# Performance work log

Hardware: AMD Instinct MI355X
Metric: run time of the kernel (lower is better)

Reference implementation:

```python
import jax, jax.numpy as jnp
import numpy as np

BN_EPS = 1e-5
NN_CHUNK = 1024  # unknown points processed per distance-matrix tile


def _batch_ids(cnt, total):
    # contiguous per-batch layout -> batch id of each point via cumsum/searchsorted
    return jnp.searchsorted(jnp.cumsum(cnt), jnp.arange(total), side='right')


def three_nn(unknown, known, ub_id, kb_id):
    """Ragged brute-force 3-NN. Returns (squared dists [N,3], global idx [N,3])."""
    N = unknown.shape[0]
    nchunk = N // NN_CHUNK
    u = unknown.reshape(nchunk, NN_CHUNK, 3)
    ub = ub_id.reshape(nchunk, NN_CHUNK)

    def body(args):
        uc, bc = args
        d2 = jnp.sum((uc[:, None, :] - known[None, :, :]) ** 2, axis=-1)  # [chunk, M]
        d2 = jnp.where(bc[:, None] == kb_id[None, :], d2, jnp.inf)  # mask cross-batch pairs
        neg_d, idx = jax.lax.top_k(-d2, 3)
        return -neg_d, idx

    d2, idx = jax.lax.map(body, (u, ub))
    return d2.reshape(N, 3), idx.reshape(N, 3)


def three_interpolate(known_feats, idx, weight):
    # gather [N,3,C] then inverse-distance weighted sum -> [N,C]
    gathered = known_feats[idx]  # [N,3,C]
    return jnp.einsum('nkc,nk->nc', gathered, weight)


def conv_bn_relu(x, W, gamma, beta):
    # 1x1 Conv2d over [1,C,N,1] == pointwise matmul; BN (training stats) over points
    h = x @ W.T  # [N, C_out]
    mean = jnp.mean(h, axis=0)
    var = jnp.mean((h - mean) ** 2, axis=0)  # biased, as torch BN normalization
    h = (h - mean) * jax.lax.rsqrt(var + BN_EPS) * gamma + beta
    return jax.nn.relu(h)


def setup_inputs() -> dict:
    key = jax.random.key(0)
    ks = jax.random.split(key, 10)
    B, Nper, Mper, C1, C2 = 4, 16384, 4096, 128, 256
    N, M = B * Nper, B * Mper
    unknown = jax.random.normal(ks[0], (N, 3), jnp.float32) * 10.0
    known = jax.random.normal(ks[1], (M, 3), jnp.float32) * 10.0
    unknown_feats = jax.random.normal(ks[2], (N, C1), jnp.float32)
    known_feats = jax.random.normal(ks[3], (M, C2), jnp.float32)
    unknown_batch_cnt = jnp.full((B,), Nper, jnp.int32)
    known_batch_cnt = jnp.full((B,), Mper, jnp.int32)
    Cin = C1 + C2  # 384
    W1 = jax.random.normal(ks[4], (256, Cin), jnp.float32) * (1.0 / np.sqrt(Cin))
    W2 = jax.random.normal(ks[5], (256, 256), jnp.float32) * (1.0 / np.sqrt(256))
    g1 = jnp.ones((256,), jnp.float32); b1 = jnp.zeros((256,), jnp.float32)
    g2 = jnp.ones((256,), jnp.float32); b2 = jnp.zeros((256,), jnp.float32)
    return {"unknown": unknown, "unknown_batch_cnt": unknown_batch_cnt,
            "known": known, "known_batch_cnt": known_batch_cnt,
            "unknown_feats": unknown_feats, "known_feats": known_feats,
            "W1": W1, "g1": g1, "b1": b1, "W2": W2, "g2": g2, "b2": b2}


def reference(unknown, unknown_batch_cnt, known, known_batch_cnt,
              unknown_feats, known_feats, W1, g1, b1, W2, g2, b2):
    ub_id = _batch_ids(unknown_batch_cnt, unknown.shape[0])
    kb_id = _batch_ids(known_batch_cnt, known.shape[0])
    dist, idx = three_nn(unknown, known, ub_id, kb_id)  # squared dists, as CUDA kernel
    dist_recip = 1.0 / (dist + 1e-8)
    weight = dist_recip / jnp.sum(dist_recip, axis=-1, keepdims=True)
    interpolated = three_interpolate(known_feats, idx, weight)  # [N, C2]
    new_features = jnp.concatenate([interpolated, unknown_feats], axis=1)  # [N, C2+C1]
    new_features = conv_bn_relu(new_features, W1, g1, b1)
    new_features = conv_bn_relu(new_features, W2, g2, b2)
    return new_features  # [N, 256]
```

## Files before the change

### kernel.cpp

```cpp
#include <hip/hip_runtime.h>
#include <math.h>

typedef __attribute__((ext_vector_type(8))) short short8;
typedef __attribute__((ext_vector_type(4))) float f32x4;

#define INF 3.0e38f
#define BN_EPS 1e-5f

__device__ __forceinline__ unsigned short f2bf(float x) {
    union { float f; unsigned u; } v; v.f = x;
    unsigned r = v.u + 0x7FFF + ((v.u >> 16) & 1);
    return (unsigned short)(r >> 16);
}
__device__ __forceinline__ float bf2f(unsigned short u) {
    return __uint_as_float(((unsigned)u) << 16);
}

__global__ __launch_bounds__(256) void knn3_kernel(
    const float* __restrict__ unk, const float* __restrict__ kn,
    const int* __restrict__ ucnt, const int* __restrict__ kcnt,
    int B, int N, float* __restrict__ wgt, int* __restrict__ idxo)
{
    __shared__ float md[4][64][3];
    __shared__ float d2g[64];
    __shared__ unsigned long long mk[4][64][3];

    int tid = threadIdx.x;
    int s = __builtin_amdgcn_readfirstlane(tid >> 6);
    int lane = tid & 63;
    int pbase = blockIdx.x * 64;
    int p = pbase + lane;

    int cum = 0, bb = 0;
    for (int i = 0; i < B; i++) { int c = ucnt[i]; if (pbase >= cum) bb = i; cum += c; }
    int kstart = 0;
    for (int i = 0; i < bb; i++) kstart += kcnt[i];
    int kend = kstart + kcnt[bb];

    float ux = unk[p * 3 + 0], uy = unk[p * 3 + 1], uz = unk[p * 3 + 2];

    int qlen = (kend - kstart) >> 2;
    int jbase = kstart + s * qlen;
    const float* kq = kn + (size_t)jbase * 3;

    float d0 = INF, d1 = INF, d2 = INF;
    auto upd = [&](float e) {
        float m0 = fmaxf(e, d0);
        float m1 = fmaxf(e, d1);
        d0 = fminf(e, d0);
        d1 = fminf(m0, d1);
        d2 = fminf(m1, d2);
    };

    for (int i = 0; i < qlen; i += 8) {
        float e[8];
#pragma unroll
        for (int c = 0; c < 8; c++) {
            float kx = kq[(i + c) * 3 + 0];
            float ky = kq[(i + c) * 3 + 1];
            float kz = kq[(i + c) * 3 + 2];
            float dx = kx - ux, dy = ky - uy, dz = kz - uz;
            e[c] = __builtin_fmaf(dx, dx, __builtin_fmaf(dy, dy, dz * dz));
        }
#pragma unroll
        for (int c = 0; c < 8; c++) upd(e[c]);
    }

    md[s][lane][0] = d0; md[s][lane][1] = d1; md[s][lane][2] = d2;
    __syncthreads();
    if (tid < 64) {
        float v0 = INF, v1 = INF, v2 = INF;
#pragma unroll
        for (int w = 0; w < 4; w++)
#pragma unroll
            for (int k = 0; k < 3; k++) {
                float e = md[w][tid][k];
                float m0 = fmaxf(e, v0);
                float m1 = fmaxf(e, v1);
                v0 = fminf(e, v0);
                v1 = fminf(m0, v1);
                v2 = fminf(m1, v2);
            }
        d2g[tid] = v2;
    }
    __syncthreads();
    float thr = d2g[lane];

    unsigned long long s0 = ~0ULL, s1 = ~0ULL, s2 = ~0ULL;
    auto insK = [&](unsigned long long k) {
        bool c0 = k < s0;
        unsigned long long t0 = c0 ? k : s0;
        unsigned long long t1 = c0 ? s0 : k;
        bool c1 = t1 < s1;
        unsigned long long u0 = c1 ? t1 : s1;
        unsigned long long u1 = c1 ? s1 : t1;
        s0 = t0; s1 = u0;
        s2 = u1 < s2 ? u1 : s2;
    };
    auto mkkey = [](float e, int gj) {
        return ((unsigned long long)__float_as_uint(e) << 32) | (unsigned)gj;
    };

    for (int i = 0; i < qlen; i += 4) {
        float e[4];
#pragma unroll
        for (int c = 0; c < 4; c++) {
            float kx = kq[(i + c) * 3 + 0];
            float ky = kq[(i + c) * 3 + 1];
            float kz = kq[(i + c) * 3 + 2];
            float dx = kx - ux, dy = ky - uy, dz = kz - uz;
            e[c] = __builtin_fmaf(dx, dx, __builtin_fmaf(dy, dy, dz * dz));
        }
        float m4 = fminf(fminf(e[0], e[1]), fminf(e[2], e[3]));
        if (m4 <= thr) {
            int gj = jbase + i;
            insK(mkkey(e[0], gj + 0));
            insK(mkkey(e[1], gj + 1));
            insK(mkkey(e[2], gj + 2));
            insK(mkkey(e[3], gj + 3));
        }
    }

    mk[s][lane][0] = s0; mk[s][lane][1] = s1; mk[s][lane][2] = s2;
    __syncthreads();

    if (tid < 64) {
        s0 = s1 = s2 = ~0ULL;
#pragma unroll
        for (int qq = 0; qq < 4; qq++)
#pragma unroll
            for (int kk = 0; kk < 3; kk++)
                insK(mk[qq][tid][kk]);

        float dd0 = __uint_as_float((unsigned)(s0 >> 32));
        float dd1 = __uint_as_float((unsigned)(s1 >> 32));
        float dd2 = __uint_as_float((unsigned)(s2 >> 32));
        float r0 = 1.0f / (dd0 + 1e-8f);
        float r1 = 1.0f / (dd1 + 1e-8f);
        float r2 = 1.0f / (dd2 + 1e-8f);
        float rs = 1.0f / (r0 + r1 + r2);
        int pp = pbase + tid;
        wgt[pp * 3 + 0] = r0 * rs;
        wgt[pp * 3 + 1] = r1 * rs;
        wgt[pp * 3 + 2] = r2 * rs;
        idxo[pp * 3 + 0] = (int)(unsigned)s0;
        idxo[pp * 3 + 1] = (int)(unsigned)s1;
        idxo[pp * 3 + 2] = (int)(unsigned)s2;
    }
}

__global__ __launch_bounds__(256) void wconv_kernel(
    const float* __restrict__ W1, const float* __restrict__ W2,
    unsigned short* __restrict__ W1b, unsigned short* __restrict__ W2b,
    int n1, int n2)
{
    int i = blockIdx.x * 256 + threadIdx.x;
    if (i < n1) W1b[i] = f2bf(W1[i]);
    int j = i - n1;
    if (j >= 0 && j < n2) W2b[j] = f2bf(W2[j]);
}

template <int K, int MODE>
__global__ __launch_bounds__(256) void gemm_bf16_kernel(
    const void* __restrict__ Aa, const float* __restrict__ ufeat,
    const unsigned short* __restrict__ W,
    const float* __restrict__ wgt, const int* __restrict__ idxv,
    const float* __restrict__ bnsum, const float* __restrict__ bnsq,
    const float* __restrict__ bng, const float* __restrict__ bnb, float invN,
    void* __restrict__ Cv, float* __restrict__ gsum, float* __restrict__ gsq)
{
    __shared__ unsigned short As[128 * 40];
    __shared__ unsigned short Bs[128 * 40];
    __shared__ float colsum[128];
    __shared__ float colsq[128];
    __shared__ float sc[256], sh[256];

    int tid = threadIdx.x;
    int w = tid >> 6, lane = tid & 63;
    int r = w >> 1, cq = w & 1;
    int m16 = lane & 15, q = lane >> 4;
    int bm = blockIdx.x * 128, bn = blockIdx.y * 128;

    if (MODE == 1) {
        float mean = bnsum[tid] * invN;
        float var = bnsq[tid] * invN - mean * mean;
        float scv = bng[tid] * rsqrtf(var + BN_EPS);
        sc[tid] = scv;
        sh[tid] = bnb[tid] - mean * scv;
    }

    int srow = tid >> 2;
    int kc = (tid & 3) * 8;
    float w0a[2], w1a[2], w2a[2];
    int j0a[2], j1a[2], j2a[2];
    if (MODE == 2) {
#pragma unroll
        for (int t = 0; t < 2; t++) {
            int pp = bm + srow + 64 * t;
            w0a[t] = wgt[pp * 3 + 0]; w1a[t] = wgt[pp * 3 + 1]; w2a[t] = wgt[pp * 3 + 2];
            j0a[t] = idxv[pp * 3 + 0]; j1a[t] = idxv[pp * 3 + 1]; j2a[t] = idxv[pp * 3 + 2];
        }
    }

    f32x4 acc[4][4];
#pragma unroll
    for (int i = 0; i < 4; i++)
#pragma unroll
        for (int j = 0; j < 4; j++) acc[i][j] = (f32x4){0.f, 0.f, 0.f, 0.f};

#pragma unroll
    for (int k0 = 0; k0 < K; k0 += 32) {
        __syncthreads();
#pragma unroll
        for (int t = 0; t < 2; t++) {
            int row = srow + 64 * t;
            int c = k0 + kc;
            ushort4 o0, o1;
            if (MODE == 2) {
                if (c < 256) {
                    const float* f0 = (const float*)Aa + (size_t)j0a[t] * 256 + c;
                    const float* f1 = (const float*)Aa + (size_t)j1a[t] * 256 + c;
                    const float* f2 = (const float*)Aa + (size_t)j2a[t] * 256 + c;
                    float4 x0 = *(const float4*)f0, x1 = *(const float4*)(f0 + 4);
                    float4 y0 = *(const float4*)f1, y1 = *(const float4*)(f1 + 4);
                    float4 z0 = *(const float4*)f2, z1 = *(const float4*)(f2 + 4);
                    float W0 = w0a[t], W1 = w1a[t], W2 = w2a[t];
                    o0.x = f2bf(x0.x * W0 + y0.x * W1 + z0.x * W2);
                    o0.y = f2bf(x0.y * W0 + y0.y * W1 + z0.y * W2);
                    o0.z = f2bf(x0.z * W0 + y0.z * W1 + z0.z * W2);
                    o0.w = f2bf(x0.w * W0 + y0.w * W1 + z0.w * W2);
                    o1.x = f2bf(x1.x * W0 + y1.x * W1 + z1.x * W2);
                    o1.y = f2bf(x1.y * W0 + y1.y * W1 + z1.y * W2);
                    o1.z = f2bf(x1.z * W0 + y1.z * W1 + z1.z * W2);
                    o1.w = f2bf(x1.w * W0 + y1.w * W1 + z1.w * W2);
                } else {
                    const float* fu = ufeat + (size_t)(bm + row) * 128 + (c - 256);
                    float4 u0 = *(const float4*)fu, u1 = *(const float4*)(fu + 4);
                    o0.x = f2bf(u0.x); o0.y = f2bf(u0.y);
                    o0.z = f2bf(u0.z); o0.w = f2bf(u0.w);
                    o1.x = f2bf(u1.x); o1.y = f2bf(u1.y);
                    o1.z = f2bf(u1.z); o1.w = f2bf(u1.w);
                }
            } else {
                const unsigned short* Ab = (const unsigned short*)Aa;
                ushort4 h0 = *(const ushort4*)(Ab + (size_t)(bm + row) * K + c);
                ushort4 h1v = *(const ushort4*)(Ab + (size_t)(bm + row) * K + c + 4);
                float4 s0 = *(const float4*)&sc[c];
                float4 s1 = *(const float4*)&sc[c + 4];
                float4 t0 = *(const float4*)&sh[c];
                float4 t1 = *(const float4*)&sh[c + 4];
                o0.x = f2bf(fmaxf(bf2f(h0.x) * s0.x + t0.x, 0.f));
                o0.y = f2bf(fmaxf(bf2f(h0.y) * s0.y + t0.y, 0.f));
                o0.z = f2bf(fmaxf(bf2f(h0.z) * s0.z + t0.z, 0.f));
                o0.w = f2bf(fmaxf(bf2f(h0.w) * s0.w + t0.w, 0.f));
                o1.x = f2bf(fmaxf(bf2f(h1v.x) * s1.x + t1.x, 0.f));
                o1.y = f2bf(fmaxf(bf2f(h1v.y) * s1.y + t1.y, 0.f));
                o1.z = f2bf(fmaxf(bf2f(h1v.z) * s1.z + t1.z, 0.f));
                o1.w = f2bf(fmaxf(bf2f(h1v.w) * s1.w + t1.w, 0.f));
            }
            *(ushort4*)&As[row * 40 + kc] = o0;
            *(ushort4*)&As[row * 40 + kc + 4] = o1;
            *(short8*)&Bs[row * 40 + kc] =
                *(const short8*)(W + (size_t)(bn + row) * K + k0 + kc);
        }
        __syncthreads();

        short8 af[4], bf[4];
#pragma unroll
        for (int sub = 0; sub < 4; sub++) {
            af[sub] = *(const short8*)&As[(r * 64 + sub * 16 + m16) * 40 + q * 8];
            bf[sub] = *(const short8*)&Bs[(cq * 64 + sub * 16 + m16) * 40 + q * 8];
        }
#pragma unroll
        for (int sm = 0; sm < 4; sm++)
#pragma unroll
            for (int sn = 0; sn < 4; sn++)
                acc[sm][sn] = __builtin_amdgcn_mfma_f32_16x16x32_bf16(
                    af[sm], bf[sn], acc[sm][sn], 0, 0, 0);
    }

    int row0 = bm + r * 64 + q * 4;
    int col0 = bn + cq * 64 + m16;
#pragma unroll
    for (int sm = 0; sm < 4; sm++)
#pragma unroll
        for (int sn = 0; sn < 4; sn++) {
            f32x4 v = acc[sm][sn];
#pragma unroll
            for (int reg = 0; reg < 4; reg++) {
                size_t idx = (size_t)(row0 + sm * 16 + reg) * 256 + col0 + sn * 16;
                if (MODE == 2) ((unsigned short*)Cv)[idx] = f2bf(v[reg]);
                else           ((float*)Cv)[idx] = v[reg];
            }
        }

    __syncthreads();
    if (tid < 128) { colsum[tid] = 0.f; colsq[tid] = 0.f; }
    __syncthreads();
#pragma unroll
    for (int sn = 0; sn < 4; sn++) {
        float sacc = 0.f, qacc = 0.f;
#pragma unroll
        for (int sm = 0; sm < 4; sm++) {
            f32x4 v = acc[sm][sn];
#pragma unroll
            for (int reg = 0; reg < 4; reg++) {
                sacc += v[reg];
                qacc += v[reg] * v[reg];
            }
        }
        int lc = cq * 64 + sn * 16 + m16;
        atomicAdd(&colsum[lc], sacc);
        atomicAdd(&colsq[lc], qacc);
    }
    __syncthreads();
    if (tid < 128) {
        atomicAdd(&gsum[bn + tid], colsum[tid]);
        atomicAdd(&gsq[bn + tid], colsq[tid]);
    }
}

__global__ __launch_bounds__(256) void final_act_kernel(
    const float* __restrict__ h2, const float* __restrict__ bnsum,
    const float* __restrict__ bnsq, const float* __restrict__ bng,
    const float* __restrict__ bnb, float invN,
    float* __restrict__ out, int total4)
{
    __shared__ float sc[256], sh[256];
    int c = threadIdx.x;
    float mean = bnsum[c] * invN;
    float var = bnsq[c] * invN - mean * mean;
    float scv = bng[c] * rsqrtf(var + BN_EPS);
    sc[c] = scv;
    sh[c] = bnb[c] - mean * scv;
    __syncthreads();

    int i = blockIdx.x * 256 + threadIdx.x;
    if (i >= total4) return;
    int c4 = i & 63;
    float4 v = ((const float4*)h2)[i];
    float4 s = *(const float4*)&sc[c4 * 4];
    float4 t = *(const float4*)&sh[c4 * 4];
    float4 o;
    o.x = fmaxf(v.x * s.x + t.x, 0.0f);
    o.y = fmaxf(v.y * s.y + t.y, 0.0f);
    o.z = fmaxf(v.z * s.z + t.z, 0.0f);
    o.w = fmaxf(v.w * s.w + t.w, 0.0f);
    ((float4*)out)[i] = o;
}

extern "C" void kernel_launch(void* const* d_in, const int* in_sizes, int n_in,
                              void* d_out, int out_size, void* d_ws, size_t ws_size,
                              hipStream_t stream)
{
    const float* unknown = (const float*)d_in[0];
    const int*   ucnt    = (const int*)d_in[1];
    const float* known   = (const float*)d_in[2];
    const int*   kcnt    = (const int*)d_in[3];
    const float* ufeat   = (const float*)d_in[4];
    const float* kfeat   = (const float*)d_in[5];
    const float* W1      = (const float*)d_in[6];
    const float* g1      = (const float*)d_in[7];
    const float* b1      = (const float*)d_in[8];
    const float* W2      = (const float*)d_in[9];
    const float* g2      = (const float*)d_in[10];
    const float* b2      = (const float*)d_in[11];

    int N = in_sizes[0] / 3;
    int B = in_sizes[1];

    char* ws = (char*)d_ws;
    size_t off = 0;
    float* wgt = (float*)(ws + off);            off += (size_t)N * 3 * 4;
    int*   idxb = (int*)(ws + off);             off += (size_t)N * 3 * 4;
    float* stats = (float*)(ws + off);          off += 4 * 256 * 4;
    float* sum1 = stats,        *sq1 = stats + 256;
    float* sum2 = stats + 512,  *sq2 = stats + 768;
    unsigned short* W1b = (unsigned short*)(ws + off);  off += 256 * 384 * 2;
    unsigned short* W2b = (unsigned short*)(ws + off);  off += 256 * 256 * 2;
    off = (off + 255) & ~(size_t)255;
    unsigned short* h1 = (unsigned short*)(ws + off);   off += (size_t)N * 256 * 2;
    off = (off + 255) & ~(size_t)255;
    float* h2 = (float*)(ws + off);

    float invN = 1.0f / (float)N;

    hipMemsetAsync(stats, 0, 4 * 256 * 4, stream);

    wconv_kernel<<<(256 * 384 + 256 * 256 + 255) / 256, 256, 0, stream>>>(
        W1, W2, W1b, W2b, 256 * 384, 256 * 256);
    knn3_kernel<<<N / 64, 256, 0, stream>>>(unknown, known, ucnt, kcnt,
                                            B, N, wgt, idxb);
    gemm_bf16_kernel<384, 2><<<dim3(N / 128, 2), 256, 0, stream>>>(
        kfeat, ufeat, W1b, wgt, idxb,
        nullptr, nullptr, nullptr, nullptr, 0.f, h1, sum1, sq1);
    gemm_bf16_kernel<256, 1><<<dim3(N / 128, 2), 256, 0, stream>>>(
        h1, nullptr, W2b, nullptr, nullptr,
        sum1, sq1, g1, b1, invN, h2, sum2, sq2);
    final_act_kernel<<<N / 4, 256, 0, stream>>>(h2, sum2, sq2, g2, b2, invN,
                                                (float*)d_out, N * 64);
}
```

Before: 393.0 us.

## Replace brute-force 3-NN with x-sorted bucket search and pruned sweep

Known points are bucketed by x coordinate per batch through a histogram, a prefix scan and an atomic scatter into a sorted float4 array. Each query then sweeps outward left and right from its bucket using four lanes, pruning once the x-distance exceeds the current third-best bound, which is shared among the lanes by shuffles. This replaces the two full brute-force passes over every known point in the batch. It adds three small kernels and divergent while loops, and the bucket range is hardcoded to [-64, 64], so points outside it are clamped into the edge buckets.

```diff
diff --git a/kernel.cpp b/kernel.cpp
--- a/kernel.cpp
+++ b/kernel.cpp
@@ -6,6 +6,12 @@
 
 #define INF 3.0e38f
 #define BN_EPS 1e-5f
+
+#define NB 1024
+#define XMIN (-64.0f)
+#define XMAX (64.0f)
+#define BW 0.125f
+#define INVW 8.0f
 
 __device__ __forceinline__ unsigned short f2bf(float x) {
     union { float f; unsigned u; } v; v.f = x;
@@ -16,125 +22,153 @@
     return __uint_as_float(((unsigned)u) << 16);
 }
 
-__global__ __launch_bounds__(256) void knn3_kernel(
-    const float* __restrict__ unk, const float* __restrict__ kn,
-    const int* __restrict__ ucnt, const int* __restrict__ kcnt,
-    int B, int N, float* __restrict__ wgt, int* __restrict__ idxo)
-{
-    __shared__ float md[4][64][3];
-    __shared__ float d2g[64];
-    __shared__ unsigned long long mk[4][64][3];
-
+__global__ __launch_bounds__(256) void hist_kernel(
+    const float* __restrict__ kn, const int* __restrict__ kcnt,
+    int B, int M, int* __restrict__ cnt)
+{
+    int j = blockIdx.x * 256 + threadIdx.x;
+    if (j >= M) return;
+    int cum = 0, bb = 0;
+    for (int i = 0; i < B; i++) { int c = kcnt[i]; if (j >= cum) bb = i; cum += c; }
+    float x = kn[j * 3];
+    int bi = (int)((x - XMIN) * INVW);
+    bi = min(max(bi, 0), NB - 1);
+    atomicAdd(&cnt[bb * NB + bi], 1);
+}
+
+__global__ __launch_bounds__(1024) void scan_kernel(
+    const int* __restrict__ cnt, int* __restrict__ bs, int* __restrict__ cur, int T)
+{
+    __shared__ int ts[1024];
     int tid = threadIdx.x;
-    int s = __builtin_amdgcn_readfirstlane(tid >> 6);
-    int lane = tid & 63;
+    int base = tid * 4;
+    int v0 = 0, v1 = 0, v2 = 0, v3 = 0;
+    if (base + 0 < T) v0 = cnt[base + 0];
+    if (base + 1 < T) v1 = cnt[base + 1];
+    if (base + 2 < T) v2 = cnt[base + 2];
+    if (base + 3 < T) v3 = cnt[base + 3];
+    int s = v0 + v1 + v2 + v3;
+    ts[tid] = s;
+    __syncthreads();
+    for (int off = 1; off < 1024; off <<= 1) {
+        int t = (tid >= off) ? ts[tid - off] : 0;
+        __syncthreads();
+        ts[tid] += t;
+        __syncthreads();
+    }
+    int ex = ts[tid] - s;
+    if (base + 0 < T) { bs[base + 0] = ex; cur[base + 0] = ex; } ex += v0;
+    if (base + 1 < T) { bs[base + 1] = ex; cur[base + 1] = ex; } ex += v1;
+    if (base + 2 < T) { bs[base + 2] = ex; cur[base + 2] = ex; } ex += v2;
+    if (base + 3 < T) { bs[base + 3] = ex; cur[base + 3] = ex; } ex += v3;
+    if (tid == ((T - 1) >> 2)) bs[T] = ts[tid];
+}
+
+__global__ __launch_bounds__(256) void scatter_kernel(
+    const float* __restrict__ kn, const int* __restrict__ kcnt,
+    int B, int M, int* __restrict__ cur, float4* __restrict__ scat)
+{
+    int j = blockIdx.x * 256 + threadIdx.x;
+    if (j >= M) return;
+    int cum = 0, bb = 0;
+    for (int i = 0; i < B; i++) { int c = kcnt[i]; if (j >= cum) bb = i; cum += c; }
+    float x = kn[j * 3], y = kn[j * 3 + 1], z = kn[j * 3 + 2];
+    int bi = (int)((x - XMIN) * INVW);
+    bi = min(max(bi, 0), NB - 1);
+    int pos = atomicAdd(&cur[bb * NB + bi], 1);
+    scat[pos] = make_float4(x, y, z, __int_as_float(j));
+}
+
+__global__ __launch_bounds__(256) void knn3_grid_kernel(
+    const float* __restrict__ unk, const int* __restrict__ ucnt,
+    const int* __restrict__ bs, const float4* __restrict__ scat,
+    int B, float* __restrict__ wgt, int* __restrict__ idxo)
+{
+    __shared__ unsigned long long mk[64][4][3];
+
+    int tid = threadIdx.x;
+    int lp = tid >> 2;
+    int role = tid & 3;
     int pbase = blockIdx.x * 64;
-    int p = pbase + lane;
+    int p = pbase + lp;
 
     int cum = 0, bb = 0;
     for (int i = 0; i < B; i++) { int c = ucnt[i]; if (pbase >= cum) bb = i; cum += c; }
-    int kstart = 0;
-    for (int i = 0; i < bb; i++) kstart += kcnt[i];
-    int kend = kstart + kcnt[bb];
 
     float ux = unk[p * 3 + 0], uy = unk[p * 3 + 1], uz = unk[p * 3 + 2];
 
-    int qlen = (kend - kstart) >> 2;
-    int jbase = kstart + s * qlen;
-    const float* kq = kn + (size_t)jbase * 3;
-
-    float d0 = INF, d1 = INF, d2 = INF;
-    auto upd = [&](float e) {
-        float m0 = fmaxf(e, d0);
-        float m1 = fmaxf(e, d1);
-        d0 = fminf(e, d0);
-        d1 = fminf(m0, d1);
-        d2 = fminf(m1, d2);
+    int kst = bs[bb * NB];
+    int ken = bs[(bb + 1) * NB];
+    int bq = (int)((ux - XMIN) * INVW);
+    bq = min(max(bq, 0), NB - 1);
+    int sp = bs[bb * NB + bq];
+
+    bool left = (role < 2);
+    int sub = role & 1;
+    int pos = left ? (sp - 1 - sub) : (sp + sub);
+    int step = left ? -2 : 2;
+
+    unsigned long long k0 = ~0ULL, k1 = ~0ULL, k2 = ~0ULL;
+    auto insK = [&](unsigned long long k) {
+        bool c0 = k < k0;
+        unsigned long long t0 = c0 ? k : k0;
+        unsigned long long t1 = c0 ? k0 : k;
+        bool c1 = t1 < k1;
+        unsigned long long u0 = c1 ? t1 : k1;
+        unsigned long long u1 = c1 ? k1 : t1;
+        k0 = t0; k1 = u0;
+        k2 = u1 < k2 ? u1 : k2;
     };
 
-    for (int i = 0; i < qlen; i += 8) {
-        float e[8];
-#pragma unroll
-        for (int c = 0; c < 8; c++) {
-            float kx = kq[(i + c) * 3 + 0];
-            float ky = kq[(i + c) * 3 + 1];
-            float kz = kq[(i + c) * 3 + 2];
-            float dx = kx - ux, dy = ky - uy, dz = kz - uz;
-            e[c] = __builtin_fmaf(dx, dx, __builtin_fmaf(dy, dy, dz * dz));
-        }
-#pragma unroll
-        for (int c = 0; c < 8; c++) upd(e[c]);
-    }
-
-    md[s][lane][0] = d0; md[s][lane][1] = d1; md[s][lane][2] = d2;
-    __syncthreads();
+    float Bnd = INF;
+    bool alive = left ? (pos >= kst) : (pos < ken);
+    int it = 0;
+    while (__any(alive)) {
+        if (alive) {
+            float4 f = scat[pos];
+            float dx = f.x - ux, dy = f.y - uy, dz = f.z - uz;
+            float e = __builtin_fmaf(dx, dx, __builtin_fmaf(dy, dy, dz * dz));
+            if (e <= Bnd) {
+                insK(((unsigned long long)__float_as_uint(e) << 32) |
+                     (unsigned)__float_as_int(f.w));
+                Bnd = fminf(Bnd, __uint_as_float((unsigned)(k2 >> 32)));
+            }
+            float xc = left ? fmaxf(f.x, XMIN) : fminf(f.x, XMAX);
+            float t = (left ? (ux - xc) : (xc - ux)) - BW;
+            if (t > 0.0f && t * t >= Bnd) alive = false;
+            pos += step;
+            if (left ? (pos < kst) : (pos >= ken)) alive = false;
+        }
+        if ((++it & 7) == 0) {
+            float b = fminf(Bnd, __shfl_xor(Bnd, 1));
+            Bnd = fminf(b, __shfl_xor(b, 2));
+        }
+    }
+
+    mk[lp][role][0] = k0; mk[lp][role][1] = k1; mk[lp][role][2] = k2;
+    __syncthreads();
+
     if (tid < 64) {
-        float v0 = INF, v1 = INF, v2 = INF;
-#pragma unroll
-        for (int w = 0; w < 4; w++)
-#pragma unroll
-            for (int k = 0; k < 3; k++) {
-                float e = md[w][tid][k];
-                float m0 = fmaxf(e, v0);
-                float m1 = fmaxf(e, v1);
-                v0 = fminf(e, v0);
-                v1 = fminf(m0, v1);
-                v2 = fminf(m1, v2);
-            }
-        d2g[tid] = v2;
-    }
-    __syncthreads();
-    float thr = d2g[lane];
-
-    unsigned long long s0 = ~0ULL, s1 = ~0ULL, s2 = ~0ULL;
-    auto insK = [&](unsigned long long k) {
-        bool c0 = k < s0;
-        unsigned long long t0 = c0 ? k : s0;
-        unsigned long long t1 = c0 ? s0 : k;
-        bool c1 = t1 < s1;
-        unsigned long long u0 = c1 ? t1 : s1;
-        unsigned long long u1 = c1 ? s1 : t1;
-        s0 = t0; s1 = u0;
-        s2 = u1 < s2 ? u1 : s2;
-    };
-    auto mkkey = [](float e, int gj) {
-        return ((unsigned long long)__float_as_uint(e) << 32) | (unsigned)gj;
-    };
-
-    for (int i = 0; i < qlen; i += 4) {
-        float e[4];
-#pragma unroll
-        for (int c = 0; c < 4; c++) {
-            float kx = kq[(i + c) * 3 + 0];
-            float ky = kq[(i + c) * 3 + 1];
-            float kz = kq[(i + c) * 3 + 2];
-            float dx = kx - ux, dy = ky - uy, dz = kz - uz;
-            e[c] = __builtin_fmaf(dx, dx, __builtin_fmaf(dy, dy, dz * dz));
-        }
-        float m4 = fminf(fminf(e[0], e[1]), fminf(e[2], e[3]));
-        if (m4 <= thr) {
-            int gj = jbase + i;
-            insK(mkkey(e[0], gj + 0));
-            insK(mkkey(e[1], gj + 1));
-            insK(mkkey(e[2], gj + 2));
-            insK(mkkey(e[3], gj + 3));
-        }
-    }
-
-    mk[s][lane][0] = s0; mk[s][lane][1] = s1; mk[s][lane][2] = s2;
-    __syncthreads();
-
-    if (tid < 64) {
-        s0 = s1 = s2 = ~0ULL;
-#pragma unroll
-        for (int qq = 0; qq < 4; qq++)
+        unsigned long long a0 = ~0ULL, a1 = ~0ULL, a2 = ~0ULL;
+        auto ins2 = [&](unsigned long long k) {
+            bool c0 = k < a0;
+            unsigned long long t0 = c0 ? k : a0;
+            unsigned long long t1 = c0 ? a0 : k;
+            bool c1 = t1 < a1;
+            unsigned long long u0 = c1 ? t1 : a1;
+            unsigned long long u1 = c1 ? a1 : t1;
+            a0 = t0; a1 = u0;
+            a2 = u1 < a2 ? u1 : a2;
+        };
+#pragma unroll
+        for (int r = 0; r < 4; r++)
 #pragma unroll
             for (int kk = 0; kk < 3; kk++)
-                insK(mk[qq][tid][kk]);
-
-        float dd0 = __uint_as_float((unsigned)(s0 >> 32));
-        float dd1 = __uint_as_float((unsigned)(s1 >> 32));
-        float dd2 = __uint_as_float((unsigned)(s2 >> 32));
+                ins2(mk[tid][r][kk]);
+
+        float dd0 = __uint_as_float((unsigned)(a0 >> 32));
+        float dd1 = __uint_as_float((unsigned)(a1 >> 32));
+        float dd2 = __uint_as_float((unsigned)(a2 >> 32));
         float r0 = 1.0f / (dd0 + 1e-8f);
         float r1 = 1.0f / (dd1 + 1e-8f);
         float r2 = 1.0f / (dd2 + 1e-8f);
@@ -143,9 +177,9 @@
         wgt[pp * 3 + 0] = r0 * rs;
         wgt[pp * 3 + 1] = r1 * rs;
         wgt[pp * 3 + 2] = r2 * rs;
-        idxo[pp * 3 + 0] = (int)(unsigned)s0;
-        idxo[pp * 3 + 1] = (int)(unsigned)s1;
-        idxo[pp * 3 + 2] = (int)(unsigned)s2;
+        idxo[pp * 3 + 0] = (int)(unsigned)a0;
+        idxo[pp * 3 + 1] = (int)(unsigned)a1;
+        idxo[pp * 3 + 2] = (int)(unsigned)a2;
     }
 }
 
@@ -368,6 +402,7 @@
 
     int N = in_sizes[0] / 3;
     int B = in_sizes[1];
+    int M = in_sizes[2] / 3;
 
     char* ws = (char*)d_ws;
     size_t off = 0;
@@ -376,8 +411,13 @@
     float* stats = (float*)(ws + off);          off += 4 * 256 * 4;
     float* sum1 = stats,        *sq1 = stats + 256;
     float* sum2 = stats + 512,  *sq2 = stats + 768;
+    int* cnt = (int*)(ws + off);                off += (size_t)B * NB * 4;
+    int* bsg = (int*)(ws + off);                off += ((size_t)B * NB + 1) * 4;
+    int* cur = (int*)(ws + off);                off += (size_t)B * NB * 4;
     unsigned short* W1b = (unsigned short*)(ws + off);  off += 256 * 384 * 2;
     unsigned short* W2b = (unsigned short*)(ws + off);  off += 256 * 256 * 2;
+    off = (off + 255) & ~(size_t)255;
+    float4* scat = (float4*)(ws + off);         off += (size_t)M * sizeof(float4);
     off = (off + 255) & ~(size_t)255;
     unsigned short* h1 = (unsigned short*)(ws + off);   off += (size_t)N * 256 * 2;
     off = (off + 255) & ~(size_t)255;
@@ -385,12 +425,17 @@
 
     float invN = 1.0f / (float)N;
 
-    hipMemsetAsync(stats, 0, 4 * 256 * 4, stream);
+    hipMemsetAsync(stats, 0, 4 * 256 * 4 + (size_t)B * NB * 4, stream);
 
     wconv_kernel<<<(256 * 384 + 256 * 256 + 255) / 256, 256, 0, stream>>>(
         W1, W2, W1b, W2b, 256 * 384, 256 * 256);
-    knn3_kernel<<<N / 64, 256, 0, stream>>>(unknown, known, ucnt, kcnt,
-                                            B, N, wgt, idxb);
+
+    hist_kernel<<<(M + 255) / 256, 256, 0, stream>>>(known, kcnt, B, M, cnt);
+    scan_kernel<<<1, 1024, 0, stream>>>(cnt, bsg, cur, B * NB);
+    scatter_kernel<<<(M + 255) / 256, 256, 0, stream>>>(known, kcnt, B, M, cur, scat);
+    knn3_grid_kernel<<<N / 64, 256, 0, stream>>>(unknown, ucnt, bsg, scat,
+                                                 B, wgt, idxb);
+
     gemm_bf16_kernel<384, 2><<<dim3(N / 128, 2), 256, 0, stream>>>(
         kfeat, ufeat, W1b, wgt, idxb,
         nullptr, nullptr, nullptr, nullptr, 0.f, h1, sum1, sq1);
```

Measured after the change: 770.3 us. 1.96x slower.
